# Kernel optimization log

Measured on AMD Instinct MI355X. Metric: run time of the kernel, lower is better.

The kernel has to match this reference:

```python
import jax, jax.numpy as jnp
import numpy as np

B, S_IN, S_PR, E, HID = 1024, 256, 128, 3, 512
PE_CH = S_IN  # PositionalEncoding1D(channels=input_depth)


def pos_enc(seq_len, channels, out_ch):
    # positional_encodings.PositionalEncoding1D: sin/cos table of width `channels`,
    # then sliced to the tensor's actual channel count (here 3).
    pos = jnp.arange(seq_len, dtype=jnp.float32)
    inv_freq = 1.0 / (10000.0 ** (jnp.arange(0, channels, 2, dtype=jnp.float32) / channels))
    ang = pos[:, None] * inv_freq[None, :]  # [seq, channels//2]
    emb = jnp.concatenate([jnp.sin(ang), jnp.cos(ang)], axis=-1)  # [seq, channels]
    return emb[:, :out_ch]


def _ln(x, w, b, eps=1e-5):
    # LayerNorm over normalized_shape=(seq, 3): normalize jointly over last two dims
    m = jnp.mean(x, axis=(-2, -1), keepdims=True)
    v = jnp.var(x, axis=(-2, -1), keepdims=True)
    return (x - m) * jax.lax.rsqrt(v + eps) * w + b


def _mha(q_in, kv_in, in_w, in_b, out_w, out_b, mask=None):
    # torch.nn.MultiheadAttention with embed_dim=3, num_heads=1, batch_first=True
    wq, wk, wv = in_w[:E], in_w[E:2 * E], in_w[2 * E:]
    q = q_in @ wq.T + in_b[:E]
    k = kv_in @ wk.T + in_b[E:2 * E]
    v = kv_in @ wv.T + in_b[2 * E:]
    scores = jnp.einsum('bqd,bkd->bqk', q, k) / jnp.sqrt(jnp.float32(E))
    if mask is not None:
        scores = scores + mask  # float attn_mask is ADDITIVE in torch MHA (tril of ones, faithful)
    attn = jax.nn.softmax(scores, axis=-1)
    o = jnp.einsum('bqk,bkd->bqd', attn, v)
    return o @ out_w.T + out_b


def _forward(X, T,
             enc_in_w, enc_in_b, enc_out_w, enc_out_b, enc_ln1_w, enc_ln1_b,
             enc_lin1_w, enc_lin1_b, enc_lin2_w, enc_lin2_b, enc_ln2_w, enc_ln2_b,
             dec_a1_in_w, dec_a1_in_b, dec_a1_out_w, dec_a1_out_b, dec_ln1_w, dec_ln1_b,
             dec_a2_in_w, dec_a2_in_b, dec_a2_out_w, dec_a2_out_b,
             dec_lin1_w, dec_lin1_b, dec_lin2_w, dec_lin2_b, dec_ln3_w, dec_ln3_b):
    p_X = X + pos_enc(S_IN, PE_CH, E)
    p_T = T + pos_enc(S_PR, PE_CH, E)
    # ---- encoder ----
    a = _mha(p_X, p_X, enc_in_w, enc_in_b, enc_out_w, enc_out_b)
    x2 = _ln(a + p_X, enc_ln1_w, enc_ln1_b)
    h = jax.nn.relu(x2 @ enc_lin1_w.T + enc_lin1_b) @ enc_lin2_w.T + enc_lin2_b
    enc_out = _ln(h + x2, enc_ln2_w, enc_ln2_b)
    # ---- decoder ----
    mask = jnp.tril(jnp.ones((S_PR, S_PR), jnp.float32))  # float mask -> additive (original bug kept)
    a = _mha(p_T, p_T, dec_a1_in_w, dec_a1_in_b, dec_a1_out_w, dec_a1_out_b, mask)
    x2 = _ln(a + p_T, dec_ln1_w, dec_ln1_b)
    a = _mha(x2, enc_out, dec_a2_in_w, dec_a2_in_b, dec_a2_out_w, dec_a2_out_b)
    x3 = _ln(a + x2, dec_ln1_w, dec_ln1_b)  # original reuses norm_1 here (norm_2 unused)
    h = jax.nn.relu(x3 @ dec_lin1_w.T + dec_lin1_b) @ dec_lin2_w.T + dec_lin2_b
    return _ln(h + x3, dec_ln3_w, dec_ln3_b)


def setup_inputs() -> dict:
    key = jax.random.key(0)
    ks = jax.random.split(key, 16)

    def rn(k, shape, s=0.1):
        return jax.random.normal(k, shape, jnp.float32) * s

    f32 = jnp.float32
    inp = {}
    inp['X'] = jax.random.normal(ks[0], (B, S_IN, E), f32)
    inp['T'] = jax.random.normal(ks[1], (B, S_PR, E), f32)
    inp['enc_in_w'] = rn(ks[2], (3 * E, E)); inp['enc_in_b'] = jnp.zeros((3 * E,), f32)
    inp['enc_out_w'] = rn(ks[3], (E, E)); inp['enc_out_b'] = jnp.zeros((E,), f32)
    inp['enc_ln1_w'] = jnp.ones((S_IN, E), f32); inp['enc_ln1_b'] = jnp.zeros((S_IN, E), f32)
    inp['enc_lin1_w'] = rn(ks[4], (HID, E)); inp['enc_lin1_b'] = jnp.zeros((HID,), f32)
    inp['enc_lin2_w'] = rn(ks[5], (E, HID)); inp['enc_lin2_b'] = jnp.zeros((E,), f32)
    inp['enc_ln2_w'] = jnp.ones((S_IN, E), f32); inp['enc_ln2_b'] = jnp.zeros((S_IN, E), f32)
    inp['dec_a1_in_w'] = rn(ks[6], (3 * E, E)); inp['dec_a1_in_b'] = jnp.zeros((3 * E,), f32)
    inp['dec_a1_out_w'] = rn(ks[7], (E, E)); inp['dec_a1_out_b'] = jnp.zeros((E,), f32)
    inp['dec_ln1_w'] = jnp.ones((S_PR, E), f32); inp['dec_ln1_b'] = jnp.zeros((S_PR, E), f32)
    inp['dec_a2_in_w'] = rn(ks[8], (3 * E, E)); inp['dec_a2_in_b'] = jnp.zeros((3 * E,), f32)
    inp['dec_a2_out_w'] = rn(ks[9], (E, E)); inp['dec_a2_out_b'] = jnp.zeros((E,), f32)
    inp['dec_lin1_w'] = rn(ks[10], (HID, E)); inp['dec_lin1_b'] = jnp.zeros((HID,), f32)
    inp['dec_lin2_w'] = rn(ks[11], (E, HID)); inp['dec_lin2_b'] = jnp.zeros((E,), f32)
    inp['dec_ln3_w'] = jnp.ones((S_PR, E), f32); inp['dec_ln3_b'] = jnp.zeros((S_PR, E), f32)
    return inp


def reference(X, T,
              enc_in_w, enc_in_b, enc_out_w, enc_out_b, enc_ln1_w, enc_ln1_b,
              enc_lin1_w, enc_lin1_b, enc_lin2_w, enc_lin2_b, enc_ln2_w, enc_ln2_b,
              dec_a1_in_w, dec_a1_in_b, dec_a1_out_w, dec_a1_out_b, dec_ln1_w, dec_ln1_b,
              dec_a2_in_w, dec_a2_in_b, dec_a2_out_w, dec_a2_out_b,
              dec_lin1_w, dec_lin1_b, dec_lin2_w, dec_lin2_b, dec_ln3_w, dec_ln3_b):
    return _forward(X, T,
                    enc_in_w, enc_in_b, enc_out_w, enc_out_b, enc_ln1_w, enc_ln1_b,
                    enc_lin1_w, enc_lin1_b, enc_lin2_w, enc_lin2_b, enc_ln2_w, enc_ln2_b,
                    dec_a1_in_w, dec_a1_in_b, dec_a1_out_w, dec_a1_out_b, dec_ln1_w, dec_ln1_b,
                    dec_a2_in_w, dec_a2_in_b, dec_a2_out_w, dec_a2_out_b,
                    dec_lin1_w, dec_lin1_b, dec_lin2_w, dec_lin2_b, dec_ln3_w, dec_ln3_b)
```

## Files before the change

kernel.cpp:

```cpp
#include <hip/hip_runtime.h>

#define NB   1024
#define SINQ 256
#define SPRQ 128
#define HIDQ 512

#define PEF1  0.93057207f
#define PEF2  0.86596438f
#define LOG2E 1.44269504089f
#define QS    0.83298066476f

typedef _Float16 h2 __attribute__((ext_vector_type(2)));

#if defined(__has_builtin) && __has_builtin(__builtin_amdgcn_exp2f)
#define EXP2(x) __builtin_amdgcn_exp2f(x)
#else
#define EXP2(x) exp2f(x)
#endif

#if defined(__has_builtin) && __has_builtin(__builtin_amdgcn_fdot2)
#define FDOT2(a, b, c) __builtin_amdgcn_fdot2((a), (b), (c), false)
#else
__device__ __forceinline__ float fdot2_sw(h2 a, h2 b, float c) {
  return fmaf((float)a.x, (float)b.x, fmaf((float)a.y, (float)b.y, c));
}
#define FDOT2(a, b, c) fdot2_sw((a), (b), (c))
#endif

__device__ __forceinline__ unsigned pk16(float a, float b) {
  h2 v; v.x = (_Float16)a; v.y = (_Float16)b;
  return __builtin_bit_cast(unsigned, v);
}
__device__ __forceinline__ h2 uph(unsigned u) { return __builtin_bit_cast(h2, u); }

__device__ __forceinline__ h2 relu2(h2 z) {
#if defined(__has_builtin) && __has_builtin(__builtin_elementwise_max)
  h2 zz; zz.x = (_Float16)0.f; zz.y = (_Float16)0.f;
  return __builtin_elementwise_max(z, zz);
#else
  z.x = z.x > (_Float16)0.f ? z.x : (_Float16)0.f;
  z.y = z.y > (_Float16)0.f ? z.y : (_Float16)0.f;
  return z;
#endif
}

__device__ __forceinline__ float sel4(float a, float b, float c, float d, int s) {
  float r = a;
  r = (s == 1) ? b : r;
  r = (s == 2) ? c : r;
  r = (s == 3) ? d : r;
  return r;
}
__device__ __forceinline__ float sel2(float a, float b, int s) {
  return s ? b : a;
}

#define C4(v) { v += __shfl_xor((v), 1, 64); v += __shfl_xor((v), 2, 64); }

__device__ __forceinline__ void block_stats(float s1, float s2, float* sRed,
                                            int tid, float nelem,
                                            float& mean, float& rstd) {
#pragma unroll
  for (int off = 32; off > 0; off >>= 1) {
    s1 += __shfl_xor(s1, off, 64);
    s2 += __shfl_xor(s2, off, 64);
  }
  __syncthreads();
  if ((tid & 63) == 0) {
    sRed[((tid >> 6) << 1) + 0] = s1;
    sRed[((tid >> 6) << 1) + 1] = s2;
  }
  __syncthreads();
  float t1 = sRed[0] + sRed[2] + sRed[4] + sRed[6];
  float t2 = sRed[1] + sRed[3] + sRed[5] + sRed[7];
  mean = t1 / nelem;
  rstd = rsqrtf(t2 / nelem - mean * mean + 1e-5f);
}

__global__ __launch_bounds__(256) void pack_tabs(
    const float* __restrict__ ew1, const float* __restrict__ eb1,
    const float* __restrict__ ew2,
    const float* __restrict__ dw1, const float* __restrict__ db1,
    const float* __restrict__ dw2,
    uint4* __restrict__ fE, uint4* __restrict__ fD, float4* __restrict__ pe)
{
  const int t = threadIdx.x;
  const int k0 = 2 * t, k1 = 2 * t + 1;
  fE[2 * t] = make_uint4(pk16(ew1[3 * k0], ew1[3 * k1]),
                         pk16(ew1[3 * k0 + 1], ew1[3 * k1 + 1]),
                         pk16(ew1[3 * k0 + 2], ew1[3 * k1 + 2]),
                         pk16(eb1[k0], eb1[k1]));
  fE[2 * t + 1] = make_uint4(pk16(ew2[k0], ew2[k1]),
                             pk16(ew2[HIDQ + k0], ew2[HIDQ + k1]),
                             pk16(ew2[2 * HIDQ + k0], ew2[2 * HIDQ + k1]), 0u);
  fD[2 * t] = make_uint4(pk16(dw1[3 * k0], dw1[3 * k1]),
                         pk16(dw1[3 * k0 + 1], dw1[3 * k1 + 1]),
                         pk16(dw1[3 * k0 + 2], dw1[3 * k1 + 2]),
                         pk16(db1[k0], db1[k1]));
  fD[2 * t + 1] = make_uint4(pk16(dw2[k0], dw2[k1]),
                             pk16(dw2[HIDQ + k0], dw2[HIDQ + k1]),
                             pk16(dw2[2 * HIDQ + k0], dw2[2 * HIDQ + k1]), 0u);
  const float p = (float)t;
  pe[t] = make_float4(sinf(p), sinf(p * PEF1), sinf(p * PEF2), 0.f);
}

__global__ __launch_bounds__(256, 4) void fused_fwd(
    const float* __restrict__ X, const float* __restrict__ T,
    const float* __restrict__ einw, const float* __restrict__ einb,
    const float* __restrict__ eow,  const float* __restrict__ eob,
    const float* __restrict__ eln1w, const float* __restrict__ eln1b,
    const float* __restrict__ eb2,
    const float* __restrict__ eln2w, const float* __restrict__ eln2b,
    const float* __restrict__ a1w, const float* __restrict__ a1b,
    const float* __restrict__ a1ow, const float* __restrict__ a1ob,
    const float* __restrict__ dln1w, const float* __restrict__ dln1b,
    const float* __restrict__ a2w, const float* __restrict__ a2b,
    const float* __restrict__ a2ow, const float* __restrict__ a2ob,
    const float* __restrict__ db2,
    const float* __restrict__ dln3w, const float* __restrict__ dln3b,
    const uint4* __restrict__ fE, const uint4* __restrict__ fD,
    const float4* __restrict__ pe,
    float* __restrict__ out)
{
  __shared__ uint4 sFE[2 * 256];
  __shared__ uint4 sFD[2 * 256];
  __shared__ uint2 sEP[SINQ];
  __shared__ uint2 sDP[SPRQ];
  __shared__ uint2 sCE[SINQ];
  __shared__ float sRed[8];

  const int b = blockIdx.x;
  const int t = threadIdx.x;
  const int lane = t & 63;
  const int s = t & 3;
  const int g = t >> 2;

  sFE[t] = fE[t]; sFE[t + 256] = fE[t + 256];
  sFD[t] = fD[t]; sFD[t + 256] = fD[t + 256];
  {
    const float4 peT = pe[t];
    const float* xr = X + (size_t)b * SINQ * 3 + 3 * t;
    sEP[t] = make_uint2(pk16(xr[0] + peT.x, xr[1] + peT.y),
                        pk16(xr[2] + peT.z, 1.f));
    if (t < SPRQ) {
      const float* tr = T + (size_t)b * SPRQ * 3 + 3 * t;
      sDP[t] = make_uint2(pk16(tr[0] + peT.x, tr[1] + peT.y),
                          pk16(tr[2] + peT.z, 1.f));
    }
  }
  __syncthreads();

  unsigned qa[4], qb[4];
#pragma unroll
  for (int m = 0; m < 4; ++m) {
    const uint2 pr = sEP[g + 64 * m];
    const h2 ha = uph(pr.x), hb = uph(pr.y);
    const float pp0 = (float)ha.x, pp1 = (float)ha.y, pp2 = (float)hb.x;
    const float q0 = (einw[0] * pp0 + einw[1] * pp1 + einw[2] * pp2 + einb[0]) * QS;
    const float q1 = (einw[3] * pp0 + einw[4] * pp1 + einw[5] * pp2 + einb[1]) * QS;
    const float q2 = (einw[6] * pp0 + einw[7] * pp1 + einw[8] * pp2 + einb[2]) * QS;
    const float qt0 = q0 * einw[9]  + q1 * einw[12] + q2 * einw[15];
    const float qt1 = q0 * einw[10] + q1 * einw[13] + q2 * einw[16];
    const float qt2 = q0 * einw[11] + q1 * einw[14] + q2 * einw[17];
    const float ce  = q0 * einb[3] + q1 * einb[4] + q2 * einb[5];
    qa[m] = pk16(qt0, qt1); qb[m] = pk16(qt2, ce);
  }
  const int rho = g + 64 * s;
  float pr0, pr1, pr2;
  {
    const uint2 prw = sEP[rho];
    const h2 ha = uph(prw.x), hb = uph(prw.y);
    pr0 = (float)ha.x; pr1 = (float)ha.y; pr2 = (float)hb.x;
  }

  float a0[4] = {0,0,0,0}, a1[4] = {0,0,0,0}, a2[4] = {0,0,0,0},
        dn[4] = {0,0,0,0};
  for (int jj = 0; jj < 64; ++jj) {
    const uint2 pj = sEP[4 * jj + s];
    const h2 pa = uph(pj.x), pb = uph(pj.y);
    const float f0 = (float)pa.x, f1 = (float)pa.y, f2 = (float)pb.x;
#pragma unroll
    for (int m = 0; m < 4; ++m) {
      const float sc = FDOT2(pa, uph(qa[m]), FDOT2(pb, uph(qb[m]), 0.f));
      const float e = EXP2(sc);
      dn[m] += e;
      a0[m] = fmaf(e, f0, a0[m]);
      a1[m] = fmaf(e, f1, a1[m]);
      a2[m] = fmaf(e, f2, a2[m]);
    }
  }
#pragma unroll
  for (int m = 0; m < 4; ++m) { C4(a0[m]); C4(a1[m]); C4(a2[m]); C4(dn[m]); }

  float r0, r1, r2;
  {
    const float myd = sel4(dn[0], dn[1], dn[2], dn[3], s);
    const float mya0 = sel4(a0[0], a0[1], a0[2], a0[3], s);
    const float mya1 = sel4(a1[0], a1[1], a1[2], a1[3], s);
    const float mya2 = sel4(a2[0], a2[1], a2[2], a2[3], s);
    const float rdn = 1.f / myd;
    const float u0 = mya0 * rdn, u1 = mya1 * rdn, u2 = mya2 * rdn;
    const float v0 = einw[18] * u0 + einw[19] * u1 + einw[20] * u2 + einb[6];
    const float v1 = einw[21] * u0 + einw[22] * u1 + einw[23] * u2 + einb[7];
    const float v2 = einw[24] * u0 + einw[25] * u1 + einw[26] * u2 + einb[8];
    r0 = eow[0] * v0 + eow[1] * v1 + eow[2] * v2 + eob[0] + pr0;
    r1 = eow[3] * v0 + eow[4] * v1 + eow[5] * v2 + eob[1] + pr1;
    r2 = eow[6] * v0 + eow[7] * v1 + eow[8] * v2 + eob[2] + pr2;
  }
  float mean, rstd;
  block_stats(r0 + r1 + r2, r0 * r0 + r1 * r1 + r2 * r2, sRed, t, 768.f, mean, rstd);
  const int lie = rho * 3;
  const float x20 = (r0 - mean) * rstd * eln1w[lie + 0] + eln1b[lie + 0];
  const float x21 = (r1 - mean) * rstd * eln1w[lie + 1] + eln1b[lie + 1];
  const float x22 = (r2 - mean) * rstd * eln1w[lie + 2] + eln1b[lie + 2];

  unsigned xxm[4], xym[4], xzm[4];
  {
    const unsigned xx = pk16(x20, x20), xy = pk16(x21, x21), xz = pk16(x22, x22);
    const int base = lane & ~3;
#pragma unroll
    for (int m = 0; m < 4; ++m) {
      xxm[m] = (unsigned)__shfl((int)xx, base + m, 64);
      xym[m] = (unsigned)__shfl((int)xy, base + m, 64);
      xzm[m] = (unsigned)__shfl((int)xz, base + m, 64);
    }
  }
  float c0[4] = {0,0,0,0}, c1[4] = {0,0,0,0}, c2[4] = {0,0,0,0};
  for (int jj = 0; jj < 64; ++jj) {
    const int pp = 4 * jj + s;
    const uint4 A = sFE[2 * pp];
    const uint4 B = sFE[2 * pp + 1];
    const h2 w1x = uph(A.x), w1y = uph(A.y), w1z = uph(A.z), b1h = uph(A.w);
    const h2 w2x = uph(B.x), w2y = uph(B.y), w2z = uph(B.z);
#pragma unroll
    for (int m = 0; m < 4; ++m) {
      h2 z = w1z * uph(xzm[m]) + b1h;
      z = w1y * uph(xym[m]) + z;
      z = w1x * uph(xxm[m]) + z;
      z = relu2(z);
      c0[m] = FDOT2(z, w2x, c0[m]);
      c1[m] = FDOT2(z, w2y, c1[m]);
      c2[m] = FDOT2(z, w2z, c2[m]);
    }
  }
#pragma unroll
  for (int m = 0; m < 4; ++m) { C4(c0[m]); C4(c1[m]); C4(c2[m]); }

  const float h0 = sel4(c0[0], c0[1], c0[2], c0[3], s) + eb2[0] + x20;
  const float h1 = sel4(c1[0], c1[1], c1[2], c1[3], s) + eb2[1] + x21;
  const float h2v = sel4(c2[0], c2[1], c2[2], c2[3], s) + eb2[2] + x22;
  block_stats(h0 + h1 + h2v, h0 * h0 + h1 * h1 + h2v * h2v, sRed, t, 768.f, mean, rstd);
  {
    const float e0 = (h0 - mean) * rstd * eln2w[lie + 0] + eln2b[lie + 0];
    const float e1 = (h1 - mean) * rstd * eln2w[lie + 1] + eln2b[lie + 1];
    const float e2 = (h2v - mean) * rstd * eln2w[lie + 2] + eln2b[lie + 2];
    sCE[rho] = make_uint2(pk16(e0, e1), pk16(e2, 1.f));
  }
  __syncthreads();

  const int ms = s & 1;
  const int ra = g + 64 * ms;

  unsigned dqa[2], dqb[2];
#pragma unroll
  for (int m = 0; m < 2; ++m) {
    const uint2 pr = sDP[g + 64 * m];
    const h2 ha = uph(pr.x), hb = uph(pr.y);
    const float pp0 = (float)ha.x, pp1 = (float)ha.y, pp2 = (float)hb.x;
    const float q0 = (a1w[0] * pp0 + a1w[1] * pp1 + a1w[2] * pp2 + a1b[0]) * QS;
    const float q1 = (a1w[3] * pp0 + a1w[4] * pp1 + a1w[5] * pp2 + a1b[1]) * QS;
    const float q2 = (a1w[6] * pp0 + a1w[7] * pp1 + a1w[8] * pp2 + a1b[2]) * QS;
    const float qt0 = q0 * a1w[9]  + q1 * a1w[12] + q2 * a1w[15];
    const float qt1 = q0 * a1w[10] + q1 * a1w[13] + q2 * a1w[16];
    const float qt2 = q0 * a1w[11] + q1 * a1w[14] + q2 * a1w[17];
    const float cd  = q0 * a1b[3] + q1 * a1b[4] + q2 * a1b[5];
    dqa[m] = pk16(qt0, qt1); dqb[m] = pk16(qt2, cd);
  }
  float pt0, pt1, pt2;
  {
    const uint2 prw = sDP[ra];
    const h2 ha = uph(prw.x), hb = uph(prw.y);
    pt0 = (float)ha.x; pt1 = (float)ha.y; pt2 = (float)hb.x;
  }

  float da0[2] = {0,0}, da1[2] = {0,0}, da2[2] = {0,0}, ddn[2] = {0,0};
  for (int jj = 0; jj < 32; ++jj) {
    const int j = 4 * jj + s;
    const uint2 pj = sDP[j];
    const h2 pa = uph(pj.x), pb = uph(pj.y);
    const float f0 = (float)pa.x, f1 = (float)pa.y, f2 = (float)pb.x;
#pragma unroll
    for (int m = 0; m < 2; ++m) {
      const float seed = (j <= g + 64 * m) ? LOG2E : 0.f;
      const float sc = FDOT2(pa, uph(dqa[m]), FDOT2(pb, uph(dqb[m]), seed));
      const float e = EXP2(sc);
      ddn[m] += e;
      da0[m] = fmaf(e, f0, da0[m]);
      da1[m] = fmaf(e, f1, da1[m]);
      da2[m] = fmaf(e, f2, da2[m]);
    }
  }
#pragma unroll
  for (int m = 0; m < 2; ++m) { C4(da0[m]); C4(da1[m]); C4(da2[m]); C4(ddn[m]); }
  {
    const float myd = sel2(ddn[0], ddn[1], ms);
    const float rdn = 1.f / myd;
    const float u0 = sel2(da0[0], da0[1], ms) * rdn;
    const float u1 = sel2(da1[0], da1[1], ms) * rdn;
    const float u2 = sel2(da2[0], da2[1], ms) * rdn;
    const float v0 = a1w[18] * u0 + a1w[19] * u1 + a1w[20] * u2 + a1b[6];
    const float v1 = a1w[21] * u0 + a1w[22] * u1 + a1w[23] * u2 + a1b[7];
    const float v2 = a1w[24] * u0 + a1w[25] * u1 + a1w[26] * u2 + a1b[8];
    r0 = a1ow[0] * v0 + a1ow[1] * v1 + a1ow[2] * v2 + a1ob[0] + pt0;
    r1 = a1ow[3] * v0 + a1ow[4] * v1 + a1ow[5] * v2 + a1ob[1] + pt1;
    r2 = a1ow[6] * v0 + a1ow[7] * v1 + a1ow[8] * v2 + a1ob[2] + pt2;
  }
  const int contrib = (s < 2) ? 1 : 0;
  block_stats(contrib ? r0 + r1 + r2 : 0.f,
              contrib ? r0 * r0 + r1 * r1 + r2 * r2 : 0.f, sRed, t, 384.f, mean, rstd);
  const int lid = ra * 3;
  const float dl1w0 = dln1w[lid + 0], dl1w1 = dln1w[lid + 1], dl1w2 = dln1w[lid + 2];
  const float dl1b0 = dln1b[lid + 0], dl1b1 = dln1b[lid + 1], dl1b2 = dln1b[lid + 2];
  const float x2d0 = (r0 - mean) * rstd * dl1w0 + dl1b0;
  const float x2d1 = (r1 - mean) * rstd * dl1w1 + dl1b1;
  const float x2d2 = (r2 - mean) * rstd * dl1w2 + dl1b2;

  unsigned cqa[2], cqb[2];
  {
    const int oth = (lane & ~3) + (ms ^ 1);
    const float ox0 = __shfl(x2d0, oth, 64);
    const float ox1 = __shfl(x2d1, oth, 64);
    const float ox2 = __shfl(x2d2, oth, 64);
    const float y00 = ms ? ox0 : x2d0;
    const float y01 = ms ? ox1 : x2d1;
    const float y02 = ms ? ox2 : x2d2;
    const float y10 = ms ? x2d0 : ox0;
    const float y11 = ms ? x2d1 : ox1;
    const float y12 = ms ? x2d2 : ox2;
#pragma unroll
    for (int m = 0; m < 2; ++m) {
      const float y0 = m ? y10 : y00, y1 = m ? y11 : y01, y2 = m ? y12 : y02;
      const float q0 = (a2w[0] * y0 + a2w[1] * y1 + a2w[2] * y2 + a2b[0]) * QS;
      const float q1 = (a2w[3] * y0 + a2w[4] * y1 + a2w[5] * y2 + a2b[1]) * QS;
      const float q2 = (a2w[6] * y0 + a2w[7] * y1 + a2w[8] * y2 + a2b[2]) * QS;
      const float qt0 = q0 * a2w[9]  + q1 * a2w[12] + q2 * a2w[15];
      const float qt1 = q0 * a2w[10] + q1 * a2w[13] + q2 * a2w[16];
      const float qt2 = q0 * a2w[11] + q1 * a2w[14] + q2 * a2w[17];
      const float cc  = q0 * a2b[3] + q1 * a2b[4] + q2 * a2b[5];
      cqa[m] = pk16(qt0, qt1); cqb[m] = pk16(qt2, cc);
    }
  }
  da0[0] = da0[1] = da1[0] = da1[1] = da2[0] = da2[1] = ddn[0] = ddn[1] = 0.f;
  for (int jj = 0; jj < 64; ++jj) {
    const uint2 pj = sCE[4 * jj + s];
    const h2 pa = uph(pj.x), pb = uph(pj.y);
    const float f0 = (float)pa.x, f1 = (float)pa.y, f2 = (float)pb.x;
#pragma unroll
    for (int m = 0; m < 2; ++m) {
      const float sc = FDOT2(pa, uph(cqa[m]), FDOT2(pb, uph(cqb[m]), 0.f));
      const float e = EXP2(sc);
      ddn[m] += e;
      da0[m] = fmaf(e, f0, da0[m]);
      da1[m] = fmaf(e, f1, da1[m]);
      da2[m] = fmaf(e, f2, da2[m]);
    }
  }
#pragma unroll
  for (int m = 0; m < 2; ++m) { C4(da0[m]); C4(da1[m]); C4(da2[m]); C4(ddn[m]); }
  {
    const float myd = sel2(ddn[0], ddn[1], ms);
    const float rdn = 1.f / myd;
    const float u0 = sel2(da0[0], da0[1], ms) * rdn;
    const float u1 = sel2(da1[0], da1[1], ms) * rdn;
    const float u2 = sel2(da2[0], da2[1], ms) * rdn;
    const float v0 = a2w[18] * u0 + a2w[19] * u1 + a2w[20] * u2 + a2b[6];
    const float v1 = a2w[21] * u0 + a2w[22] * u1 + a2w[23] * u2 + a2b[7];
    const float v2 = a2w[24] * u0 + a2w[25] * u1 + a2w[26] * u2 + a2b[8];
    r0 = a2ow[0] * v0 + a2ow[1] * v1 + a2ow[2] * v2 + a2ob[0] + x2d0;
    r1 = a2ow[3] * v0 + a2ow[4] * v1 + a2ow[5] * v2 + a2ob[1] + x2d1;
    r2 = a2ow[6] * v0 + a2ow[7] * v1 + a2ow[8] * v2 + a2ob[2] + x2d2;
  }
  block_stats(contrib ? r0 + r1 + r2 : 0.f,
              contrib ? r0 * r0 + r1 * r1 + r2 * r2 : 0.f, sRed, t, 384.f, mean, rstd);
  const float x30 = (r0 - mean) * rstd * dl1w0 + dl1b0;
  const float x31 = (r1 - mean) * rstd * dl1w1 + dl1b1;
  const float x32 = (r2 - mean) * rstd * dl1w2 + dl1b2;

  unsigned x3x0, x3y0, x3z0, x3x1, x3y1, x3z1;
  {
    const unsigned xx = pk16(x30, x30), xy = pk16(x31, x31), xz = pk16(x32, x32);
    const int oth = (lane & ~3) + (ms ^ 1);
    const unsigned oxx = (unsigned)__shfl((int)xx, oth, 64);
    const unsigned oxy = (unsigned)__shfl((int)xy, oth, 64);
    const unsigned oxz = (unsigned)__shfl((int)xz, oth, 64);
    x3x0 = ms ? oxx : xx; x3y0 = ms ? oxy : xy; x3z0 = ms ? oxz : xz;
    x3x1 = ms ? xx : oxx; x3y1 = ms ? xy : oxy; x3z1 = ms ? xz : oxz;
  }
  float e0[2] = {0,0}, e1[2] = {0,0}, e2[2] = {0,0};
  for (int jj = 0; jj < 64; ++jj) {
    const int pp = 4 * jj + s;
    const uint4 A = sFD[2 * pp];
    const uint4 B = sFD[2 * pp + 1];
    const h2 w1x = uph(A.x), w1y = uph(A.y), w1z = uph(A.z), b1h = uph(A.w);
    const h2 w2x = uph(B.x), w2y = uph(B.y), w2z = uph(B.z);
#pragma unroll
    for (int m = 0; m < 2; ++m) {
      h2 z = w1z * uph(m ? x3z1 : x3z0) + b1h;
      z = w1y * uph(m ? x3y1 : x3y0) + z;
      z = w1x * uph(m ? x3x1 : x3x0) + z;
      z = relu2(z);
      e0[m] = FDOT2(z, w2x, e0[m]);
      e1[m] = FDOT2(z, w2y, e1[m]);
      e2[m] = FDOT2(z, w2z, e2[m]);
    }
  }
#pragma unroll
  for (int m = 0; m < 2; ++m) { C4(e0[m]); C4(e1[m]); C4(e2[m]); }

  const float f0 = sel2(e0[0], e0[1], ms) + db2[0] + x30;
  const float f1 = sel2(e1[0], e1[1], ms) + db2[1] + x31;
  const float f2 = sel2(e2[0], e2[1], ms) + db2[2] + x32;
  block_stats(contrib ? f0 + f1 + f2 : 0.f,
              contrib ? f0 * f0 + f1 * f1 + f2 * f2 : 0.f, sRed, t, 384.f, mean, rstd);
  if (s < 2) {
    float* op = out + ((size_t)b * SPRQ + ra) * 3;
    op[0] = (f0 - mean) * rstd * dln3w[lid + 0] + dln3b[lid + 0];
    op[1] = (f1 - mean) * rstd * dln3w[lid + 1] + dln3b[lid + 1];
    op[2] = (f2 - mean) * rstd * dln3w[lid + 2] + dln3b[lid + 2];
  }
}

extern "C" void kernel_launch(void* const* d_in, const int* in_sizes, int n_in,
                              void* d_out, int out_size, void* d_ws, size_t ws_size,
                              hipStream_t stream) {
  (void)in_sizes; (void)n_in; (void)out_size; (void)ws_size;
  float* ws = (float*)d_ws;
  uint4* fE = (uint4*)ws;
  uint4* fD = (uint4*)(ws + 2048);
  float4* pe = (float4*)(ws + 4096);

  pack_tabs<<<1, 256, 0, stream>>>(
      (const float*)d_in[8],  (const float*)d_in[9],  (const float*)d_in[10],
      (const float*)d_in[24], (const float*)d_in[25], (const float*)d_in[26],
      fE, fD, pe);

  fused_fwd<<<NB, 256, 0, stream>>>(
      (const float*)d_in[0],  (const float*)d_in[1],
      (const float*)d_in[2],  (const float*)d_in[3],
      (const float*)d_in[4],  (const float*)d_in[5],
      (const float*)d_in[6],  (const float*)d_in[7],
      (const float*)d_in[11],
      (const float*)d_in[12], (const float*)d_in[13],
      (const float*)d_in[14], (const float*)d_in[15],
      (const float*)d_in[16], (const float*)d_in[17],
      (const float*)d_in[18], (const float*)d_in[19],
      (const float*)d_in[20], (const float*)d_in[21],
      (const float*)d_in[22], (const float*)d_in[23],
      (const float*)d_in[27],
      (const float*)d_in[28], (const float*)d_in[29],
      fE, fD, pe,
      (float*)d_out);
}
```

Before: 178.8 us.

## Double threads per batch block, splitting each row's key loop over eight lanes

Raises the block size from 256 to 512 threads, so each query row is served by 8 lanes instead of 4. Every inner loop (attention over keys and the FFN hidden loop) runs half as many iterations, and the partial sums are reduced with an extra xor-shuffle step. Lanes 4-7 duplicate the row-level work and are masked out of the LayerNorm statistics and stores. This adds parallelism per batch item to hide latency, at the cost of redundant per-row arithmetic, more shuffles and higher register pressure under the 512/8 launch bounds.

Measured after the change: 225.0 us. +25.8%, slower.

```diff
diff --git a/kernel.cpp b/kernel.cpp
--- a/kernel.cpp
+++ b/kernel.cpp
@@ -55,7 +55,8 @@
   return s ? b : a;
 }
 
-#define C4(v) { v += __shfl_xor((v), 1, 64); v += __shfl_xor((v), 2, 64); }
+#define C8(v) { v += __shfl_xor((v), 1, 64); v += __shfl_xor((v), 2, 64); \
+                v += __shfl_xor((v), 4, 64); }
 
 __device__ __forceinline__ void block_stats(float s1, float s2, float* sRed,
                                             int tid, float nelem,
@@ -71,8 +72,9 @@
     sRed[((tid >> 6) << 1) + 1] = s2;
   }
   __syncthreads();
-  float t1 = sRed[0] + sRed[2] + sRed[4] + sRed[6];
-  float t2 = sRed[1] + sRed[3] + sRed[5] + sRed[7];
+  float t1 = 0.f, t2 = 0.f;
+#pragma unroll
+  for (int w = 0; w < 8; ++w) { t1 += sRed[2 * w]; t2 += sRed[2 * w + 1]; }
   mean = t1 / nelem;
   rstd = rsqrtf(t2 / nelem - mean * mean + 1e-5f);
 }
@@ -104,7 +106,7 @@
   pe[t] = make_float4(sinf(p), sinf(p * PEF1), sinf(p * PEF2), 0.f);
 }
 
-__global__ __launch_bounds__(256, 4) void fused_fwd(
+__global__ __launch_bounds__(512, 8) void fused_fwd(
     const float* __restrict__ X, const float* __restrict__ T,
     const float* __restrict__ einw, const float* __restrict__ einb,
     const float* __restrict__ eow,  const float* __restrict__ eob,
@@ -122,22 +124,25 @@
     const float4* __restrict__ pe,
     float* __restrict__ out)
 {
-  __shared__ uint4 sFE[2 * 256];
-  __shared__ uint4 sFD[2 * 256];
+  __shared__ uint4 sFE[512];
+  __shared__ uint4 sFD[512];
   __shared__ uint2 sEP[SINQ];
   __shared__ uint2 sDP[SPRQ];
   __shared__ uint2 sCE[SINQ];
-  __shared__ float sRed[8];
+  __shared__ float sRed[16];
 
   const int b = blockIdx.x;
   const int t = threadIdx.x;
   const int lane = t & 63;
-  const int s = t & 3;
-  const int g = t >> 2;
-
-  sFE[t] = fE[t]; sFE[t + 256] = fE[t + 256];
-  sFD[t] = fD[t]; sFD[t + 256] = fD[t + 256];
-  {
+  const int s = t & 7;
+  const int g = t >> 3;
+  const int se = s & 3;
+  const int ms = s & 1;
+  const int base = lane & ~7;
+
+  sFE[t] = fE[t];
+  sFD[t] = fD[t];
+  if (t < SINQ) {
     const float4 peT = pe[t];
     const float* xr = X + (size_t)b * SINQ * 3 + 3 * t;
     sEP[t] = make_uint2(pk16(xr[0] + peT.x, xr[1] + peT.y),
@@ -165,7 +170,7 @@
     const float ce  = q0 * einb[3] + q1 * einb[4] + q2 * einb[5];
     qa[m] = pk16(qt0, qt1); qb[m] = pk16(qt2, ce);
   }
-  const int rho = g + 64 * s;
+  const int rho = g + 64 * se;
   float pr0, pr1, pr2;
   {
     const uint2 prw = sEP[rho];
@@ -175,8 +180,8 @@
 
   float a0[4] = {0,0,0,0}, a1[4] = {0,0,0,0}, a2[4] = {0,0,0,0},
         dn[4] = {0,0,0,0};
-  for (int jj = 0; jj < 64; ++jj) {
-    const uint2 pj = sEP[4 * jj + s];
+  for (int jj = 0; jj < 32; ++jj) {
+    const uint2 pj = sEP[8 * jj + s];
     const h2 pa = uph(pj.x), pb = uph(pj.y);
     const float f0 = (float)pa.x, f1 = (float)pa.y, f2 = (float)pb.x;
 #pragma unroll
@@ -190,14 +195,14 @@
     }
   }
 #pragma unroll
-  for (int m = 0; m < 4; ++m) { C4(a0[m]); C4(a1[m]); C4(a2[m]); C4(dn[m]); }
+  for (int m = 0; m < 4; ++m) { C8(a0[m]); C8(a1[m]); C8(a2[m]); C8(dn[m]); }
 
   float r0, r1, r2;
   {
-    const float myd = sel4(dn[0], dn[1], dn[2], dn[3], s);
-    const float mya0 = sel4(a0[0], a0[1], a0[2], a0[3], s);
-    const float mya1 = sel4(a1[0], a1[1], a1[2], a1[3], s);
-    const float mya2 = sel4(a2[0], a2[1], a2[2], a2[3], s);
+    const float myd = sel4(dn[0], dn[1], dn[2], dn[3], se);
+    const float mya0 = sel4(a0[0], a0[1], a0[2], a0[3], se);
+    const float mya1 = sel4(a1[0], a1[1], a1[2], a1[3], se);
+    const float mya2 = sel4(a2[0], a2[1], a2[2], a2[3], se);
     const float rdn = 1.f / myd;
     const float u0 = mya0 * rdn, u1 = mya1 * rdn, u2 = mya2 * rdn;
     const float v0 = einw[18] * u0 + einw[19] * u1 + einw[20] * u2 + einb[6];
@@ -207,8 +212,10 @@
     r1 = eow[3] * v0 + eow[4] * v1 + eow[5] * v2 + eob[1] + pr1;
     r2 = eow[6] * v0 + eow[7] * v1 + eow[8] * v2 + eob[2] + pr2;
   }
+  const int ec = (s < 4) ? 1 : 0;
   float mean, rstd;
-  block_stats(r0 + r1 + r2, r0 * r0 + r1 * r1 + r2 * r2, sRed, t, 768.f, mean, rstd);
+  block_stats(ec ? r0 + r1 + r2 : 0.f,
+              ec ? r0 * r0 + r1 * r1 + r2 * r2 : 0.f, sRed, t, 768.f, mean, rstd);
   const int lie = rho * 3;
   const float x20 = (r0 - mean) * rstd * eln1w[lie + 0] + eln1b[lie + 0];
   const float x21 = (r1 - mean) * rstd * eln1w[lie + 1] + eln1b[lie + 1];
@@ -217,7 +224,6 @@
   unsigned xxm[4], xym[4], xzm[4];
   {
     const unsigned xx = pk16(x20, x20), xy = pk16(x21, x21), xz = pk16(x22, x22);
-    const int base = lane & ~3;
 #pragma unroll
     for (int m = 0; m < 4; ++m) {
       xxm[m] = (unsigned)__shfl((int)xx, base + m, 64);
@@ -226,8 +232,8 @@
     }
   }
   float c0[4] = {0,0,0,0}, c1[4] = {0,0,0,0}, c2[4] = {0,0,0,0};
-  for (int jj = 0; jj < 64; ++jj) {
-    const int pp = 4 * jj + s;
+  for (int jj = 0; jj < 32; ++jj) {
+    const int pp = 8 * jj + s;
     const uint4 A = sFE[2 * pp];
     const uint4 B = sFE[2 * pp + 1];
     const h2 w1x = uph(A.x), w1y = uph(A.y), w1z = uph(A.z), b1h = uph(A.w);
@@ -244,13 +250,14 @@
     }
   }
 #pragma unroll
-  for (int m = 0; m < 4; ++m) { C4(c0[m]); C4(c1[m]); C4(c2[m]); }
-
-  const float h0 = sel4(c0[0], c0[1], c0[2], c0[3], s) + eb2[0] + x20;
-  const float h1 = sel4(c1[0], c1[1], c1[2], c1[3], s) + eb2[1] + x21;
-  const float h2v = sel4(c2[0], c2[1], c2[2], c2[3], s) + eb2[2] + x22;
-  block_stats(h0 + h1 + h2v, h0 * h0 + h1 * h1 + h2v * h2v, sRed, t, 768.f, mean, rstd);
-  {
+  for (int m = 0; m < 4; ++m) { C8(c0[m]); C8(c1[m]); C8(c2[m]); }
+
+  const float h0 = sel4(c0[0], c0[1], c0[2], c0[3], se) + eb2[0] + x20;
+  const float h1 = sel4(c1[0], c1[1], c1[2], c1[3], se) + eb2[1] + x21;
+  const float h2v = sel4(c2[0], c2[1], c2[2], c2[3], se) + eb2[2] + x22;
+  block_stats(ec ? h0 + h1 + h2v : 0.f,
+              ec ? h0 * h0 + h1 * h1 + h2v * h2v : 0.f, sRed, t, 768.f, mean, rstd);
+  if (s < 4) {
     const float e0 = (h0 - mean) * rstd * eln2w[lie + 0] + eln2b[lie + 0];
     const float e1 = (h1 - mean) * rstd * eln2w[lie + 1] + eln2b[lie + 1];
     const float e2 = (h2v - mean) * rstd * eln2w[lie + 2] + eln2b[lie + 2];
@@ -258,7 +265,6 @@
   }
   __syncthreads();
 
-  const int ms = s & 1;
   const int ra = g + 64 * ms;
 
   unsigned dqa[2], dqb[2];
@@ -284,8 +290,8 @@
   }
 
   float da0[2] = {0,0}, da1[2] = {0,0}, da2[2] = {0,0}, ddn[2] = {0,0};
-  for (int jj = 0; jj < 32; ++jj) {
-    const int j = 4 * jj + s;
+  for (int jj = 0; jj < 16; ++jj) {
+    const int j = 8 * jj + s;
     const uint2 pj = sDP[j];
     const h2 pa = uph(pj.x), pb = uph(pj.y);
     const float f0 = (float)pa.x, f1 = (float)pa.y, f2 = (float)pb.x;
@@ -301,7 +307,7 @@
     }
   }
 #pragma unroll
-  for (int m = 0; m < 2; ++m) { C4(da0[m]); C4(da1[m]); C4(da2[m]); C4(ddn[m]); }
+  for (int m = 0; m < 2; ++m) { C8(da0[m]); C8(da1[m]); C8(da2[m]); C8(ddn[m]); }
   {
     const float myd = sel2(ddn[0], ddn[1], ms);
     const float rdn = 1.f / myd;
@@ -315,9 +321,9 @@
     r1 = a1ow[3] * v0 + a1ow[4] * v1 + a1ow[5] * v2 + a1ob[1] + pt1;
     r2 = a1ow[6] * v0 + a1ow[7] * v1 + a1ow[8] * v2 + a1ob[2] + pt2;
   }
-  const int contrib = (s < 2) ? 1 : 0;
-  block_stats(contrib ? r0 + r1 + r2 : 0.f,
-              contrib ? r0 * r0 + r1 * r1 + r2 * r2 : 0.f, sRed, t, 384.f, mean, rstd);
+  const int dc = (s < 2) ? 1 : 0;
+  block_stats(dc ? r0 + r1 + r2 : 0.f,
+              dc ? r0 * r0 + r1 * r1 + r2 * r2 : 0.f, sRed, t, 384.f, mean, rstd);
   const int lid = ra * 3;
   const float dl1w0 = dln1w[lid + 0], dl1w1 = dln1w[lid + 1], dl1w2 = dln1w[lid + 2];
   const float dl1b0 = dln1b[lid + 0], dl1b1 = dln1b[lid + 1], dl1b2 = dln1b[lid + 2];
@@ -327,19 +333,11 @@
 
   unsigned cqa[2], cqb[2];
   {
-    const int oth = (lane & ~3) + (ms ^ 1);
-    const float ox0 = __shfl(x2d0, oth, 64);
-    const float ox1 = __shfl(x2d1, oth, 64);
-    const float ox2 = __shfl(x2d2, oth, 64);
-    const float y00 = ms ? ox0 : x2d0;
-    const float y01 = ms ? ox1 : x2d1;
-    const float y02 = ms ? ox2 : x2d2;
-    const float y10 = ms ? x2d0 : ox0;
-    const float y11 = ms ? x2d1 : ox1;
-    const float y12 = ms ? x2d2 : ox2;
 #pragma unroll
     for (int m = 0; m < 2; ++m) {
-      const float y0 = m ? y10 : y00, y1 = m ? y11 : y01, y2 = m ? y12 : y02;
+      const float y0 = __shfl(x2d0, base + m, 64);
+      const float y1 = __shfl(x2d1, base + m, 64);
+      const float y2 = __shfl(x2d2, base + m, 64);
       const float q0 = (a2w[0] * y0 + a2w[1] * y1 + a2w[2] * y2 + a2b[0]) * QS;
       const float q1 = (a2w[3] * y0 + a2w[4] * y1 + a2w[5] * y2 + a2b[1]) * QS;
       const float q2 = (a2w[6] * y0 + a2w[7] * y1 + a2w[8] * y2 + a2b[2]) * QS;
@@ -351,8 +349,8 @@
     }
   }
   da0[0] = da0[1] = da1[0] = da1[1] = da2[0] = da2[1] = ddn[0] = ddn[1] = 0.f;
-  for (int jj = 0; jj < 64; ++jj) {
-    const uint2 pj = sCE[4 * jj + s];
+  for (int jj = 0; jj < 32; ++jj) {
+    const uint2 pj = sCE[8 * jj + s];
     const h2 pa = uph(pj.x), pb = uph(pj.y);
     const float f0 = (float)pa.x, f1 = (float)pa.y, f2 = (float)pb.x;
 #pragma unroll
@@ -366,7 +364,7 @@
     }
   }
 #pragma unroll
-  for (int m = 0; m < 2; ++m) { C4(da0[m]); C4(da1[m]); C4(da2[m]); C4(ddn[m]); }
+  for (int m = 0; m < 2; ++m) { C8(da0[m]); C8(da1[m]); C8(da2[m]); C8(ddn[m]); }
   {
     const float myd = sel2(ddn[0], ddn[1], ms);
     const float rdn = 1.f / myd;
@@ -380,8 +378,8 @@
     r1 = a2ow[3] * v0 + a2ow[4] * v1 + a2ow[5] * v2 + a2ob[1] + x2d1;
     r2 = a2ow[6] * v0 + a2ow[7] * v1 + a2ow[8] * v2 + a2ob[2] + x2d2;
   }
-  block_stats(contrib ? r0 + r1 + r2 : 0.f,
-              contrib ? r0 * r0 + r1 * r1 + r2 * r2 : 0.f, sRed, t, 384.f, mean, rstd);
+  block_stats(dc ? r0 + r1 + r2 : 0.f,
+              dc ? r0 * r0 + r1 * r1 + r2 * r2 : 0.f, sRed, t, 384.f, mean, rstd);
   const float x30 = (r0 - mean) * rstd * dl1w0 + dl1b0;
   const float x31 = (r1 - mean) * rstd * dl1w1 + dl1b1;
   const float x32 = (r2 - mean) * rstd * dl1w2 + dl1b2;
@@ -389,16 +387,16 @@
   unsigned x3x0, x3y0, x3z0, x3x1, x3y1, x3z1;
   {
     const unsigned xx = pk16(x30, x30), xy = pk16(x31, x31), xz = pk16(x32, x32);
-    const int oth = (lane & ~3) + (ms ^ 1);
-    const unsigned oxx = (unsigned)__shfl((int)xx, oth, 64);
-    const unsigned oxy = (unsigned)__shfl((int)xy, oth, 64);
-    const unsigned oxz = (unsigned)__shfl((int)xz, oth, 64);
-    x3x0 = ms ? oxx : xx; x3y0 = ms ? oxy : xy; x3z0 = ms ? oxz : xz;
-    x3x1 = ms ? xx : oxx; x3y1 = ms ? xy : oxy; x3z1 = ms ? xz : oxz;
+    x3x0 = (unsigned)__shfl((int)xx, base + 0, 64);
+    x3y0 = (unsigned)__shfl((int)xy, base + 0, 64);
+    x3z0 = (unsigned)__shfl((int)xz, base + 0, 64);
+    x3x1 = (unsigned)__shfl((int)xx, base + 1, 64);
+    x3y1 = (unsigned)__shfl((int)xy, base + 1, 64);
+    x3z1 = (unsigned)__shfl((int)xz, base + 1, 64);
   }
   float e0[2] = {0,0}, e1[2] = {0,0}, e2[2] = {0,0};
-  for (int jj = 0; jj < 64; ++jj) {
-    const int pp = 4 * jj + s;
+  for (int jj = 0; jj < 32; ++jj) {
+    const int pp = 8 * jj + s;
     const uint4 A = sFD[2 * pp];
     const uint4 B = sFD[2 * pp + 1];
     const h2 w1x = uph(A.x), w1y = uph(A.y), w1z = uph(A.z), b1h = uph(A.w);
@@ -415,13 +413,13 @@
     }
   }
 #pragma unroll
-  for (int m = 0; m < 2; ++m) { C4(e0[m]); C4(e1[m]); C4(e2[m]); }
+  for (int m = 0; m < 2; ++m) { C8(e0[m]); C8(e1[m]); C8(e2[m]); }
 
   const float f0 = sel2(e0[0], e0[1], ms) + db2[0] + x30;
   const float f1 = sel2(e1[0], e1[1], ms) + db2[1] + x31;
   const float f2 = sel2(e2[0], e2[1], ms) + db2[2] + x32;
-  block_stats(contrib ? f0 + f1 + f2 : 0.f,
-              contrib ? f0 * f0 + f1 * f1 + f2 * f2 : 0.f, sRed, t, 384.f, mean, rstd);
+  block_stats(dc ? f0 + f1 + f2 : 0.f,
+              dc ? f0 * f0 + f1 * f1 + f2 * f2 : 0.f, sRed, t, 384.f, mean, rstd);
   if (s < 2) {
     float* op = out + ((size_t)b * SPRQ + ra) * 3;
     op[0] = (f0 - mean) * rstd * dln3w[lid + 0] + dln3b[lid + 0];
@@ -444,7 +442,7 @@
       (const float*)d_in[24], (const float*)d_in[25], (const float*)d_in[26],
       fE, fD, pe);
 
-  fused_fwd<<<NB, 256, 0, stream>>>(
+  fused_fwd<<<NB, 512, 0, stream>>>(
       (const float*)d_in[0],  (const float*)d_in[1],
       (const float*)d_in[2],  (const float*)d_in[3],
       (const float*)d_in[4],  (const float*)d_in[5],
```

## Remap decoder phase to 8-lane groups handling four query rows each

Applied to the files above, without the earlier changes.

The decoder stages (self-attention, cross-attention, FFN) now assign each group of 8 lanes four query rows instead of each group of 4 lanes two rows. Every key/weight element loaded from LDS is therefore reused across four rows, which halves the per-lane loop trip counts and the LDS reads per unit of work. The cost is more accumulator registers, an extra shuffle-reduction step, and a four-way select to pick each lane's row. Lanes with s8>=4 hold duplicate rows and are masked out of the LayerNorm statistics and the output store.

Measured after the change: 204.9 us. 14.6% more time.

```diff
diff --git a/kernel.cpp b/kernel.cpp
--- a/kernel.cpp
+++ b/kernel.cpp
@@ -51,11 +51,10 @@
   r = (s == 3) ? d : r;
   return r;
 }
-__device__ __forceinline__ float sel2(float a, float b, int s) {
-  return s ? b : a;
-}
 
 #define C4(v) { v += __shfl_xor((v), 1, 64); v += __shfl_xor((v), 2, 64); }
+#define C8(v) { v += __shfl_xor((v), 1, 64); v += __shfl_xor((v), 2, 64); \
+                v += __shfl_xor((v), 4, 64); }
 
 __device__ __forceinline__ void block_stats(float s1, float s2, float* sRed,
                                             int tid, float nelem,
@@ -258,13 +257,16 @@
   }
   __syncthreads();
 
-  const int ms = s & 1;
-  const int ra = g + 64 * ms;
-
-  unsigned dqa[2], dqb[2];
-#pragma unroll
-  for (int m = 0; m < 2; ++m) {
-    const uint2 pr = sDP[g + 64 * m];
+  const int s8 = t & 7;
+  const int g8 = t >> 3;
+  const int mo = s8 & 3;
+  const int rd = g8 + 32 * mo;
+  const int base8 = lane & ~7;
+
+  unsigned dqa[4], dqb[4];
+#pragma unroll
+  for (int m = 0; m < 4; ++m) {
+    const uint2 pr = sDP[g8 + 32 * m];
     const h2 ha = uph(pr.x), hb = uph(pr.y);
     const float pp0 = (float)ha.x, pp1 = (float)ha.y, pp2 = (float)hb.x;
     const float q0 = (a1w[0] * pp0 + a1w[1] * pp1 + a1w[2] * pp2 + a1b[0]) * QS;
@@ -278,20 +280,21 @@
   }
   float pt0, pt1, pt2;
   {
-    const uint2 prw = sDP[ra];
+    const uint2 prw = sDP[rd];
     const h2 ha = uph(prw.x), hb = uph(prw.y);
     pt0 = (float)ha.x; pt1 = (float)ha.y; pt2 = (float)hb.x;
   }
 
-  float da0[2] = {0,0}, da1[2] = {0,0}, da2[2] = {0,0}, ddn[2] = {0,0};
-  for (int jj = 0; jj < 32; ++jj) {
-    const int j = 4 * jj + s;
+  float da0[4] = {0,0,0,0}, da1[4] = {0,0,0,0}, da2[4] = {0,0,0,0},
+        ddn[4] = {0,0,0,0};
+  for (int jj = 0; jj < 16; ++jj) {
+    const int j = 8 * jj + s8;
     const uint2 pj = sDP[j];
     const h2 pa = uph(pj.x), pb = uph(pj.y);
     const float f0 = (float)pa.x, f1 = (float)pa.y, f2 = (float)pb.x;
 #pragma unroll
-    for (int m = 0; m < 2; ++m) {
-      const float seed = (j <= g + 64 * m) ? LOG2E : 0.f;
+    for (int m = 0; m < 4; ++m) {
+      const float seed = (j <= g8 + 32 * m) ? LOG2E : 0.f;
       const float sc = FDOT2(pa, uph(dqa[m]), FDOT2(pb, uph(dqb[m]), seed));
       const float e = EXP2(sc);
       ddn[m] += e;
@@ -301,13 +304,13 @@
     }
   }
 #pragma unroll
-  for (int m = 0; m < 2; ++m) { C4(da0[m]); C4(da1[m]); C4(da2[m]); C4(ddn[m]); }
-  {
-    const float myd = sel2(ddn[0], ddn[1], ms);
+  for (int m = 0; m < 4; ++m) { C8(da0[m]); C8(da1[m]); C8(da2[m]); C8(ddn[m]); }
+  {
+    const float myd = sel4(ddn[0], ddn[1], ddn[2], ddn[3], mo);
     const float rdn = 1.f / myd;
-    const float u0 = sel2(da0[0], da0[1], ms) * rdn;
-    const float u1 = sel2(da1[0], da1[1], ms) * rdn;
-    const float u2 = sel2(da2[0], da2[1], ms) * rdn;
+    const float u0 = sel4(da0[0], da0[1], da0[2], da0[3], mo) * rdn;
+    const float u1 = sel4(da1[0], da1[1], da1[2], da1[3], mo) * rdn;
+    const float u2 = sel4(da2[0], da2[1], da2[2], da2[3], mo) * rdn;
     const float v0 = a1w[18] * u0 + a1w[19] * u1 + a1w[20] * u2 + a1b[6];
     const float v1 = a1w[21] * u0 + a1w[22] * u1 + a1w[23] * u2 + a1b[7];
     const float v2 = a1w[24] * u0 + a1w[25] * u1 + a1w[26] * u2 + a1b[8];
@@ -315,48 +318,39 @@
     r1 = a1ow[3] * v0 + a1ow[4] * v1 + a1ow[5] * v2 + a1ob[1] + pt1;
     r2 = a1ow[6] * v0 + a1ow[7] * v1 + a1ow[8] * v2 + a1ob[2] + pt2;
   }
-  const int contrib = (s < 2) ? 1 : 0;
-  block_stats(contrib ? r0 + r1 + r2 : 0.f,
-              contrib ? r0 * r0 + r1 * r1 + r2 * r2 : 0.f, sRed, t, 384.f, mean, rstd);
-  const int lid = ra * 3;
+  const int dc = (s8 < 4) ? 1 : 0;
+  block_stats(dc ? r0 + r1 + r2 : 0.f,
+              dc ? r0 * r0 + r1 * r1 + r2 * r2 : 0.f, sRed, t, 384.f, mean, rstd);
+  const int lid = rd * 3;
   const float dl1w0 = dln1w[lid + 0], dl1w1 = dln1w[lid + 1], dl1w2 = dln1w[lid + 2];
   const float dl1b0 = dln1b[lid + 0], dl1b1 = dln1b[lid + 1], dl1b2 = dln1b[lid + 2];
   const float x2d0 = (r0 - mean) * rstd * dl1w0 + dl1b0;
   const float x2d1 = (r1 - mean) * rstd * dl1w1 + dl1b1;
   const float x2d2 = (r2 - mean) * rstd * dl1w2 + dl1b2;
 
-  unsigned cqa[2], cqb[2];
-  {
-    const int oth = (lane & ~3) + (ms ^ 1);
-    const float ox0 = __shfl(x2d0, oth, 64);
-    const float ox1 = __shfl(x2d1, oth, 64);
-    const float ox2 = __shfl(x2d2, oth, 64);
-    const float y00 = ms ? ox0 : x2d0;
-    const float y01 = ms ? ox1 : x2d1;
-    const float y02 = ms ? ox2 : x2d2;
-    const float y10 = ms ? x2d0 : ox0;
-    const float y11 = ms ? x2d1 : ox1;
-    const float y12 = ms ? x2d2 : ox2;
-#pragma unroll
-    for (int m = 0; m < 2; ++m) {
-      const float y0 = m ? y10 : y00, y1 = m ? y11 : y01, y2 = m ? y12 : y02;
-      const float q0 = (a2w[0] * y0 + a2w[1] * y1 + a2w[2] * y2 + a2b[0]) * QS;
-      const float q1 = (a2w[3] * y0 + a2w[4] * y1 + a2w[5] * y2 + a2b[1]) * QS;
-      const float q2 = (a2w[6] * y0 + a2w[7] * y1 + a2w[8] * y2 + a2b[2]) * QS;
-      const float qt0 = q0 * a2w[9]  + q1 * a2w[12] + q2 * a2w[15];
-      const float qt1 = q0 * a2w[10] + q1 * a2w[13] + q2 * a2w[16];
-      const float qt2 = q0 * a2w[11] + q1 * a2w[14] + q2 * a2w[17];
-      const float cc  = q0 * a2b[3] + q1 * a2b[4] + q2 * a2b[5];
-      cqa[m] = pk16(qt0, qt1); cqb[m] = pk16(qt2, cc);
-    }
-  }
-  da0[0] = da0[1] = da1[0] = da1[1] = da2[0] = da2[1] = ddn[0] = ddn[1] = 0.f;
-  for (int jj = 0; jj < 64; ++jj) {
-    const uint2 pj = sCE[4 * jj + s];
+  unsigned cqa[4], cqb[4];
+#pragma unroll
+  for (int m = 0; m < 4; ++m) {
+    const float y0 = __shfl(x2d0, base8 + m, 64);
+    const float y1 = __shfl(x2d1, base8 + m, 64);
+    const float y2 = __shfl(x2d2, base8 + m, 64);
+    const float q0 = (a2w[0] * y0 + a2w[1] * y1 + a2w[2] * y2 + a2b[0]) * QS;
+    const float q1 = (a2w[3] * y0 + a2w[4] * y1 + a2w[5] * y2 + a2b[1]) * QS;
+    const float q2 = (a2w[6] * y0 + a2w[7] * y1 + a2w[8] * y2 + a2b[2]) * QS;
+    const float qt0 = q0 * a2w[9]  + q1 * a2w[12] + q2 * a2w[15];
+    const float qt1 = q0 * a2w[10] + q1 * a2w[13] + q2 * a2w[16];
+    const float qt2 = q0 * a2w[11] + q1 * a2w[14] + q2 * a2w[17];
+    const float cc  = q0 * a2b[3] + q1 * a2b[4] + q2 * a2b[5];
+    cqa[m] = pk16(qt0, qt1); cqb[m] = pk16(qt2, cc);
+  }
+#pragma unroll
+  for (int m = 0; m < 4; ++m) { da0[m] = 0.f; da1[m] = 0.f; da2[m] = 0.f; ddn[m] = 0.f; }
+  for (int jj = 0; jj < 32; ++jj) {
+    const uint2 pj = sCE[8 * jj + s8];
     const h2 pa = uph(pj.x), pb = uph(pj.y);
     const float f0 = (float)pa.x, f1 = (float)pa.y, f2 = (float)pb.x;
 #pragma unroll
-    for (int m = 0; m < 2; ++m) {
+    for (int m = 0; m < 4; ++m) {
       const float sc = FDOT2(pa, uph(cqa[m]), FDOT2(pb, uph(cqb[m]), 0.f));
       const float e = EXP2(sc);
       ddn[m] += e;
@@ -366,13 +360,13 @@
     }
   }
 #pragma unroll
-  for (int m = 0; m < 2; ++m) { C4(da0[m]); C4(da1[m]); C4(da2[m]); C4(ddn[m]); }
-  {
-    const float myd = sel2(ddn[0], ddn[1], ms);
+  for (int m = 0; m < 4; ++m) { C8(da0[m]); C8(da1[m]); C8(da2[m]); C8(ddn[m]); }
+  {
+    const float myd = sel4(ddn[0], ddn[1], ddn[2], ddn[3], mo);
     const float rdn = 1.f / myd;
-    const float u0 = sel2(da0[0], da0[1], ms) * rdn;
-    const float u1 = sel2(da1[0], da1[1], ms) * rdn;
-    const float u2 = sel2(da2[0], da2[1], ms) * rdn;
+    const float u0 = sel4(da0[0], da0[1], da0[2], da0[3], mo) * rdn;
+    const float u1 = sel4(da1[0], da1[1], da1[2], da1[3], mo) * rdn;
+    const float u2 = sel4(da2[0], da2[1], da2[2], da2[3], mo) * rdn;
     const float v0 = a2w[18] * u0 + a2w[19] * u1 + a2w[20] * u2 + a2b[6];
     const float v1 = a2w[21] * u0 + a2w[22] * u1 + a2w[23] * u2 + a2b[7];
     const float v2 = a2w[24] * u0 + a2w[25] * u1 + a2w[26] * u2 + a2b[8];
@@ -380,34 +374,34 @@
     r1 = a2ow[3] * v0 + a2ow[4] * v1 + a2ow[5] * v2 + a2ob[1] + x2d1;
     r2 = a2ow[6] * v0 + a2ow[7] * v1 + a2ow[8] * v2 + a2ob[2] + x2d2;
   }
-  block_stats(contrib ? r0 + r1 + r2 : 0.f,
-              contrib ? r0 * r0 + r1 * r1 + r2 * r2 : 0.f, sRed, t, 384.f, mean, rstd);
+  block_stats(dc ? r0 + r1 + r2 : 0.f,
+              dc ? r0 * r0 + r1 * r1 + r2 * r2 : 0.f, sRed, t, 384.f, mean, rstd);
   const float x30 = (r0 - mean) * rstd * dl1w0 + dl1b0;
   const float x31 = (r1 - mean) * rstd * dl1w1 + dl1b1;
   const float x32 = (r2 - mean) * rstd * dl1w2 + dl1b2;
 
-  unsigned x3x0, x3y0, x3z0, x3x1, x3y1, x3z1;
+  unsigned x3x[4], x3y[4], x3z[4];
   {
     const unsigned xx = pk16(x30, x30), xy = pk16(x31, x31), xz = pk16(x32, x32);
-    const int oth = (lane & ~3) + (ms ^ 1);
-    const unsigned oxx = (unsigned)__shfl((int)xx, oth, 64);
-    const unsigned oxy = (unsigned)__shfl((int)xy, oth, 64);
-    const unsigned oxz = (unsigned)__shfl((int)xz, oth, 64);
-    x3x0 = ms ? oxx : xx; x3y0 = ms ? oxy : xy; x3z0 = ms ? oxz : xz;
-    x3x1 = ms ? xx : oxx; x3y1 = ms ? xy : oxy; x3z1 = ms ? xz : oxz;
-  }
-  float e0[2] = {0,0}, e1[2] = {0,0}, e2[2] = {0,0};
-  for (int jj = 0; jj < 64; ++jj) {
-    const int pp = 4 * jj + s;
+#pragma unroll
+    for (int m = 0; m < 4; ++m) {
+      x3x[m] = (unsigned)__shfl((int)xx, base8 + m, 64);
+      x3y[m] = (unsigned)__shfl((int)xy, base8 + m, 64);
+      x3z[m] = (unsigned)__shfl((int)xz, base8 + m, 64);
+    }
+  }
+  float e0[4] = {0,0,0,0}, e1[4] = {0,0,0,0}, e2[4] = {0,0,0,0};
+  for (int jj = 0; jj < 32; ++jj) {
+    const int pp = 8 * jj + s8;
     const uint4 A = sFD[2 * pp];
     const uint4 B = sFD[2 * pp + 1];
     const h2 w1x = uph(A.x), w1y = uph(A.y), w1z = uph(A.z), b1h = uph(A.w);
     const h2 w2x = uph(B.x), w2y = uph(B.y), w2z = uph(B.z);
 #pragma unroll
-    for (int m = 0; m < 2; ++m) {
-      h2 z = w1z * uph(m ? x3z1 : x3z0) + b1h;
-      z = w1y * uph(m ? x3y1 : x3y0) + z;
-      z = w1x * uph(m ? x3x1 : x3x0) + z;
+    for (int m = 0; m < 4; ++m) {
+      h2 z = w1z * uph(x3z[m]) + b1h;
+      z = w1y * uph(x3y[m]) + z;
+      z = w1x * uph(x3x[m]) + z;
       z = relu2(z);
       e0[m] = FDOT2(z, w2x, e0[m]);
       e1[m] = FDOT2(z, w2y, e1[m]);
@@ -415,15 +409,15 @@
     }
   }
 #pragma unroll
-  for (int m = 0; m < 2; ++m) { C4(e0[m]); C4(e1[m]); C4(e2[m]); }
-
-  const float f0 = sel2(e0[0], e0[1], ms) + db2[0] + x30;
-  const float f1 = sel2(e1[0], e1[1], ms) + db2[1] + x31;
-  const float f2 = sel2(e2[0], e2[1], ms) + db2[2] + x32;
-  block_stats(contrib ? f0 + f1 + f2 : 0.f,
-              contrib ? f0 * f0 + f1 * f1 + f2 * f2 : 0.f, sRed, t, 384.f, mean, rstd);
-  if (s < 2) {
-    float* op = out + ((size_t)b * SPRQ + ra) * 3;
+  for (int m = 0; m < 4; ++m) { C8(e0[m]); C8(e1[m]); C8(e2[m]); }
+
+  const float f0 = sel4(e0[0], e0[1], e0[2], e0[3], mo) + db2[0] + x30;
+  const float f1 = sel4(e1[0], e1[1], e1[2], e1[3], mo) + db2[1] + x31;
+  const float f2 = sel4(e2[0], e2[1], e2[2], e2[3], mo) + db2[2] + x32;
+  block_stats(dc ? f0 + f1 + f2 : 0.f,
+              dc ? f0 * f0 + f1 * f1 + f2 * f2 : 0.f, sRed, t, 384.f, mean, rstd);
+  if (s8 < 4) {
+    float* op = out + ((size_t)b * SPRQ + rd) * 3;
     op[0] = (f0 - mean) * rstd * dln3w[lid + 0] + dln3b[lid + 0];
     op[1] = (f1 - mean) * rstd * dln3w[lid + 1] + dln3b[lid + 1];
     op[2] = (f2 - mean) * rstd * dln3w[lid + 2] + dln3b[lid + 2];
```
